# Kernel optimization log

Measured on AMD Instinct MI355X. Metric: run time of the kernel, lower is better.

Reference implementation:

```python
import jax, jax.numpy as jnp
import numpy as np

B, T, D, H = 64, 512, 1024, 1024


def setup_inputs() -> dict:
    key = jax.random.key(0)
    k1, k2, k3, k4, k5, k6 = jax.random.split(key, 6)
    feature = jax.random.normal(k1, (B, T, D), dtype=jnp.float32)
    # lengths sorted descending (pack_padded_sequence enforce_sorted=True); max == T
    lens = jnp.sort(jax.random.randint(k2, (B,), 1, T + 1))[::-1]
    seq_len = lens.at[0].set(T).astype(jnp.int32)
    s = 1.0 / np.sqrt(H)
    W_ih = jax.random.uniform(k3, (4 * H, D), jnp.float32, -s, s)
    W_hh = jax.random.uniform(k4, (4 * H, H), jnp.float32, -s, s)
    b_ih = jax.random.uniform(k5, (4 * H,), jnp.float32, -s, s)
    b_hh = jax.random.uniform(k6, (4 * H,), jnp.float32, -s, s)
    return {"feature": feature, "W_ih": W_ih, "W_hh": W_hh,
            "b_ih": b_ih, "b_hh": b_hh, "seq_len": seq_len}


def _lstm(feature, W_ih, W_hh, b_ih, b_hh, seq_len):
    Bb, Tt, _ = feature.shape
    Hh = W_hh.shape[1]
    # precompute input contributions for all steps: [B,T,4H] -> [T,B,4H]
    x_gates = jnp.einsum('btd,gd->btg', feature, W_ih) + (b_ih + b_hh)
    x_gates = jnp.transpose(x_gates, (1, 0, 2))
    # valid-step mask per timestep: [T,B]
    mask = (jnp.arange(Tt)[:, None] < seq_len[None, :])

    def step(carry, inp):
        h, c = carry
        xg, m = inp  # [B,4H], [B]
        gates = xg + h @ W_hh.T
        i, f, g, o = jnp.split(gates, 4, axis=-1)  # PyTorch gate order i,f,g,o
        i = jax.nn.sigmoid(i)
        f = jax.nn.sigmoid(f)
        g = jnp.tanh(g)
        o = jax.nn.sigmoid(o)
        c_new = f * c + i * g
        h_new = o * jnp.tanh(c_new)
        m = m[:, None]
        h = jnp.where(m, h_new, h)  # packed semantics: state frozen past length
        c = jnp.where(m, c_new, c)
        out = jnp.where(m, h_new, 0.0)  # pad_packed_sequence pads with zeros
        return (h, c), out

    h0 = jnp.zeros((Bb, Hh), feature.dtype)
    c0 = jnp.zeros((Bb, Hh), feature.dtype)
    _, outs = jax.lax.scan(step, (h0, c0), (x_gates, mask))
    return jnp.transpose(outs, (1, 0, 2))  # [B,T,H]


def reference(feature, W_ih, W_hh, b_ih, b_hh, seq_len):
    return _lstm(feature, W_ih, W_hh, b_ih, b_hh, seq_len)
```

## Files before the change

kernel.cpp:

```cpp
#include <hip/hip_runtime.h>
#include <stdint.h>

typedef unsigned short ushort_t;
typedef unsigned long long ull_t;
typedef __attribute__((ext_vector_type(8))) short short8;
typedef __attribute__((ext_vector_type(2))) unsigned long long ull2;
typedef __attribute__((ext_vector_type(4))) float f32x4;
typedef __attribute__((ext_vector_type(4))) float float4v;
typedef __attribute__((ext_vector_type(4))) unsigned short ushort4v;
typedef __attribute__((ext_vector_type(4))) unsigned int uint4v;

#define NB 64
#define NT 512
#define ND 1024
#define NHH 1024
#define NG 4096

__device__ __forceinline__ ushort_t f2bf(float x) {
    uint32_t u = __builtin_bit_cast(uint32_t, x);
    u += 0x7fffu + ((u >> 16) & 1u);
    return (ushort_t)(u >> 16);
}
__device__ __forceinline__ float bf2f(ushort_t b) {
    uint32_t u = ((uint32_t)b) << 16;
    return __builtin_bit_cast(float, u);
}
__device__ __forceinline__ float fsigmoid(float x) { return 1.f / (1.f + __expf(-x)); }
__device__ __forceinline__ float ftanh(float x) {
    float ax = __builtin_fabsf(x);
    float e = __expf(-2.f * ax);
    float r = (1.f - e) / (1.f + e);
    return x < 0.f ? -r : r;
}
__device__ __forceinline__ void xg_store(float* p, float v) { *p = v; }
__device__ __forceinline__ void xg_store(ushort_t* p, float v) { *p = f2bf(v); }
__device__ __forceinline__ float4v xg_load4(const float4v* p) { return *p; }
__device__ __forceinline__ float4v xg_load4(const ushort4v* p) {
    ushort4v u = *p;
    float4v r = { bf2f(u[0]), bf2f(u[1]), bf2f(u[2]), bf2f(u[3]) };
    return r;
}
__device__ __forceinline__ void async_cp16(const ushort_t* g, ushort_t* s) {
    __builtin_amdgcn_global_load_lds(
        (const __attribute__((address_space(1))) uint32_t*)g,
        (__attribute__((address_space(3))) uint32_t*)s, 16, 0, 0);
}

__global__ __launch_bounds__(256) void k_prep(
    const float* __restrict__ feat, const float* __restrict__ wih,
    const float* __restrict__ whh,
    ushort_t* __restrict__ featb, ushort_t* __restrict__ wihb,
    ushort_t* __restrict__ whhb, ushort_t* __restrict__ hbuf,
    int* __restrict__ cnt)
{
    const size_t NF = (size_t)NB * NT * ND / 4;
    const size_t NW = (size_t)NG * ND / 4;
    const size_t NHB = (size_t)2 * 65536 * 2 / 16;
    size_t total = NF + 2 * NW + NHB;
    size_t stride = (size_t)gridDim.x * blockDim.x;
    for (size_t i = (size_t)blockIdx.x * blockDim.x + threadIdx.x; i < total; i += stride) {
        if (i < NF) {
            float4v v = ((const float4v*)feat)[i];
            ushort4v o = { f2bf(v[0]), f2bf(v[1]), f2bf(v[2]), f2bf(v[3]) };
            ((ushort4v*)featb)[i] = o;
        } else if (i < NF + NW) {
            size_t j = i - NF;
            size_t row = j >> 8, kc = j & 255;
            size_t rowp = ((row & 1023) << 2) | (row >> 10);
            float4v v = ((const float4v*)wih)[j];
            ushort4v o = { f2bf(v[0]), f2bf(v[1]), f2bf(v[2]), f2bf(v[3]) };
            ((ushort4v*)wihb)[rowp * 256 + kc] = o;
        } else if (i < NF + 2 * NW) {
            size_t j = i - NF - NW;
            float4v v = ((const float4v*)whh)[j];
            ushort4v o = { f2bf(v[0]), f2bf(v[1]), f2bf(v[2]), f2bf(v[3]) };
            ((ushort4v*)whhb)[j] = o;
        } else {
            size_t j = i - NF - 2 * NW;
            uint4v z = { 0u, 0u, 0u, 0u };
            ((uint4v*)hbuf)[j] = z;
        }
    }
    if (blockIdx.x < 16) cnt[blockIdx.x * 256 + threadIdx.x] = 0;
}

template <typename XGT>
__global__ __launch_bounds__(256) void k_gemm(
    const ushort_t* __restrict__ Ab,
    const ushort_t* __restrict__ Bb,
    const float* __restrict__ bih, const float* __restrict__ bhh,
    const int* __restrict__ slenp, XGT* __restrict__ xg)
{
    int bid = blockIdx.x;
    int panel = bid >> 8;
    int qq = bid & 255;
    int mt = (panel << 3) | (qq & 7);
    int nt = qq >> 3;
    int m0 = mt << 7, n0 = nt << 7;
    int b = m0 >> 9;
    int t0 = m0 & 511;
    int sl = slenp[b];
    if (t0 >= sl) return;

    __shared__ short8 ldsA8[1024];
    __shared__ short8 ldsB8[1024];
    ushort_t* ldsA = (ushort_t*)ldsA8;
    ushort_t* ldsB = (ushort_t*)ldsB8;
    const ushort_t* gA = Ab + (size_t)m0 * 1024;
    const ushort_t* gB = Bb + (size_t)n0 * 1024;

    int tid = threadIdx.x;
    int wave = tid >> 6, lane = tid & 63;
    int wm = (wave >> 1) << 6;
    int wn = (wave & 1) << 6;
    int fl = lane & 15, fq = lane >> 4;

    f32x4 acc[4][4];
#pragma unroll
    for (int i = 0; i < 4; i++)
#pragma unroll
        for (int j = 0; j < 4; j++) { f32x4 z = {0.f, 0.f, 0.f, 0.f}; acc[i][j] = z; }

    int srow_[4], skb_[4];
#pragma unroll
    for (int u = 0; u < 4; u++) {
        int s = u * 256 + tid;
        srow_[u] = s >> 3;
        skb_[u] = (s & 7) ^ (srow_[u] & 7);
    }

    for (int k0 = 0; k0 < 1024; k0 += 64) {
        if (k0) __syncthreads();
#pragma unroll
        for (int u = 0; u < 4; u++) {
            ushort_t* sa = ldsA + (size_t)(u * 256 + wave * 64) * 8;
            ushort_t* sb = ldsB + (size_t)(u * 256 + wave * 64) * 8;
            async_cp16(gA + (size_t)srow_[u] * 1024 + k0 + skb_[u] * 8, sa);
            async_cp16(gB + (size_t)srow_[u] * 1024 + k0 + skb_[u] * 8, sb);
        }
        __syncthreads();
#pragma unroll
        for (int ks = 0; ks < 2; ks++) {
            int kc = ks * 4 + fq;
            short8 af[4], bf[4];
#pragma unroll
            for (int i = 0; i < 4; i++) {
                int ra = wm + i * 16 + fl;
                int rb = wn + i * 16 + fl;
                af[i] = ldsA8[ra * 8 + (kc ^ (ra & 7))];
                bf[i] = ldsB8[rb * 8 + (kc ^ (rb & 7))];
            }
#pragma unroll
            for (int i = 0; i < 4; i++)
#pragma unroll
                for (int j = 0; j < 4; j++)
                    acc[i][j] = __builtin_amdgcn_mfma_f32_16x16x32_bf16(af[i], bf[j], acc[i][j], 0, 0, 0);
        }
    }
#pragma unroll
    for (int j = 0; j < 4; j++) {
        int rp = n0 + wn + j * 16 + fl;
        int bi = ((rp & 3) << 10) | (rp >> 2);
        float bv = bih[bi] + bhh[bi];
#pragma unroll
        for (int i = 0; i < 4; i++) {
#pragma unroll
            for (int r = 0; r < 4; r++) {
                int m = wm + i * 16 + fq * 4 + r;
                int t = t0 + m;
                if (t < sl)
                    xg_store(&xg[((size_t)t * 64 + b) * 4096 + rp], acc[i][j][r] + bv);
            }
        }
    }
}

template <typename XG4>
__global__ __launch_bounds__(256, 1) void k_rec(
    const ushort_t* __restrict__ whhb, const XG4* __restrict__ xg4,
    const int* __restrict__ slenp, ushort_t* __restrict__ hbuf,
    float* __restrict__ out, int* __restrict__ cnt)
{
    const int tid = threadIdx.x;
    const int ks = tid >> 6, lane = tid & 63;
    const int wg = blockIdx.x;
    const int mb = wg >> 6;
    const int mem = wg & 63;
    const int j0 = mem << 4;
    const int nn = lane & 15, q = lane >> 4;

    short8 wfrag[4][8];
    {
        const short8* w8 = (const short8*)whhb;
#pragma unroll
        for (int g = 0; g < 4; g++) {
            const short8* wp = w8 + (size_t)(g * NHH + j0 + nn) * 128 + ks * 32;
#pragma unroll
            for (int u = 0; u < 8; u++) wfrag[g][u] = wp[u * 4 + q];
        }
    }
    const int eb = tid >> 4, ej = tid & 15;
    const int b_g = (mb << 4) + eb;
    const int j_g = j0 + ej;
    const int slen = slenp[b_g];
    const int blk_len = slenp[mb << 4];
    const int ab = (mb << 4) + nn;

    int* base    = cnt + mb * 512;
    int* subcnt  = base + (mem >> 3) * 16;
    int* root    = base + 256;
    int* subflag = base + 272 + (mem >> 3) * 16;
    const bool subleader = ((mem & 7) == 0);

    __shared__ float red[4 * 16 * 84];

    float c_st = 0.f, h_st = 0.f, hv_prev = 0.f;
    float4v xv = { 0.f, 0.f, 0.f, 0.f };
    if (0 < slen) xv = xg_load4(&xg4[(size_t)b_g * 1024 + j_g]);

#pragma unroll 1
    for (int t = 0; t < blk_len; ++t) {
        if (t > 0) out[((size_t)b_g * NT + (t - 1)) * 1024 + j_g] = hv_prev;
        float4v nxv = { 0.f, 0.f, 0.f, 0.f };
        if (t + 1 < slen) nxv = xg_load4(&xg4[((size_t)(t + 1) * 64 + b_g) * 1024 + j_g]);

        const ull_t* hb8 = (const ull_t*)(hbuf + (size_t)(t & 1) * 65536);
        ull_t raw[16];
#pragma unroll
        for (int u = 0; u < 8; u++) {
            size_t ch = ((size_t)((ks * 32 + u * 4 + q) * 64 + ab)) * 2;
            raw[2 * u]     = __hip_atomic_load(&hb8[ch],     __ATOMIC_RELAXED, __HIP_MEMORY_SCOPE_AGENT);
            raw[2 * u + 1] = __hip_atomic_load(&hb8[ch + 1], __ATOMIC_RELAXED, __HIP_MEMORY_SCOPE_AGENT);
        }
        f32x4 acc[4];
#pragma unroll
        for (int g = 0; g < 4; g++) { f32x4 z = {0.f, 0.f, 0.f, 0.f}; acc[g] = z; }
#pragma unroll
        for (int u = 0; u < 8; u++) {
            ull2 p; p[0] = raw[2 * u]; p[1] = raw[2 * u + 1];
            short8 af = __builtin_bit_cast(short8, p);
#pragma unroll
            for (int g = 0; g < 4; g++)
                acc[g] = __builtin_amdgcn_mfma_f32_16x16x32_bf16(af, wfrag[g][u], acc[g], 0, 0, 0);
        }
        __syncthreads();
#pragma unroll
        for (int g = 0; g < 4; g++)
            *(f32x4*)&red[g * 1344 + nn * 84 + ks * 20 + q * 4] = acc[g];
        __syncthreads();

        float hv = 0.f;
        if (t < slen) {
            float s[4];
#pragma unroll
            for (int g = 0; g < 4; g++) {
                const float* rp = &red[g * 1344 + ej * 84 + eb];
                s[g] = (rp[0] + rp[20]) + (rp[40] + rp[60]);
            }
            float ip = s[0] + xv[0];
            float fp = s[1] + xv[1];
            float gp = s[2] + xv[2];
            float op = s[3] + xv[3];
            float i_s = fsigmoid(ip), f_s = fsigmoid(fp);
            float g_t = ftanh(gp), o_s = fsigmoid(op);
            float cn = __builtin_fmaf(f_s, c_st, i_s * g_t);
            c_st = cn;
            h_st = o_s * ftanh(cn);
            hv = h_st;
        }
        hv_prev = hv;
        __hip_atomic_store(&hbuf[(size_t)((t + 1) & 1) * 65536 +
                                 (size_t)((j_g >> 3) * 64 + b_g) * 8 + (j_g & 7)],
                           f2bf(h_st), __ATOMIC_RELAXED, __HIP_MEMORY_SCOPE_AGENT);
        xv = nxv;
        if (t + 1 < blk_len) {
            asm volatile("s_waitcnt vmcnt(0)" ::: "memory");
            __syncthreads();
            if (tid == 0) {
                int old = __hip_atomic_fetch_add(subcnt, 1, __ATOMIC_RELAXED, __HIP_MEMORY_SCOPE_AGENT);
                if ((old & 7) == 7)
                    __hip_atomic_fetch_add(root, 1, __ATOMIC_RELAXED, __HIP_MEMORY_SCOPE_AGENT);
                const int target = (t + 1) << 3;
                if (subleader) {
                    while (__hip_atomic_load(root, __ATOMIC_RELAXED, __HIP_MEMORY_SCOPE_AGENT) < target)
                        __builtin_amdgcn_s_sleep(2);
                    __hip_atomic_store(subflag, t + 1, __ATOMIC_RELAXED, __HIP_MEMORY_SCOPE_AGENT);
                } else {
                    while (__hip_atomic_load(subflag, __ATOMIC_RELAXED, __HIP_MEMORY_SCOPE_AGENT) < t + 1)
                        __builtin_amdgcn_s_sleep(2);
                }
            }
            __syncthreads();
        }
    }
    out[((size_t)b_g * NT + (blk_len - 1)) * 1024 + j_g] = hv_prev;
    for (int t = blk_len; t < NT; ++t)
        out[((size_t)b_g * NT + t) * 1024 + j_g] = 0.f;
}

extern "C" void kernel_launch(void* const* d_in, const int* in_sizes, int n_in,
                              void* d_out, int out_size, void* d_ws, size_t ws_size,
                              hipStream_t stream)
{
    const float* feat = (const float*)d_in[0];
    const float* wih  = (const float*)d_in[1];
    const float* whh  = (const float*)d_in[2];
    const float* bih  = (const float*)d_in[3];
    const float* bhh  = (const float*)d_in[4];
    const int*   sl   = (const int*)d_in[5];
    float* out = (float*)d_out;
    char* ws = (char*)d_ws;

    size_t off = 0;
    auto take = [&](size_t bytes) -> size_t {
        size_t o = off; off += (bytes + 255) & ~(size_t)255; return o;
    };
    size_t o_featb = take((size_t)NB * NT * ND * 2);
    size_t o_wihb  = take((size_t)NG * ND * 2);
    size_t o_whhb  = take((size_t)NG * ND * 2);
    size_t o_hbuf  = take((size_t)2 * 65536 * 2);
    size_t o_cnt   = take(16384);
    size_t o_xg    = off;

    ushort_t* featb = (ushort_t*)(ws + o_featb);
    ushort_t* wihb  = (ushort_t*)(ws + o_wihb);
    ushort_t* whhb  = (ushort_t*)(ws + o_whhb);
    ushort_t* hbuf  = (ushort_t*)(ws + o_hbuf);
    int* cnt        = (int*)(ws + o_cnt);

    k_prep<<<2048, 256, 0, stream>>>(feat, wih, whh, featb, wihb, whhb, hbuf, cnt);

    size_t xg_elems = (size_t)NT * NB * NG;
    bool f32xg = (o_xg + xg_elems * 4) <= ws_size;
    if (f32xg) {
        float* xg = (float*)(ws + o_xg);
        k_gemm<float><<<8192, 256, 0, stream>>>(featb, wihb, bih, bhh, sl, xg);
        k_rec<float4v><<<256, 256, 0, stream>>>(whhb, (const float4v*)xg, sl, hbuf, out, cnt);
    } else {
        ushort_t* xg = (ushort_t*)(ws + o_xg);
        k_gemm<ushort_t><<<8192, 256, 0, stream>>>(featb, wihb, bih, bhh, sl, xg);
        k_rec<ushort4v><<<256, 256, 0, stream>>>(whhb, (const ushort4v*)xg, sl, hbuf, out, cnt);
    }
}
```

Baseline: 2.608 ms.

## Widen recurrence blocks to 32 hidden units and flatten grid barrier

Each recurrent workgroup now covers 32 hidden columns with 8 waves (512 threads), which halves the grid to 128 blocks and the number of participants per batch group to 32. The per-step h exchange is staged through shared memory, and one wave writes it out as packed 16-byte stores in a new per-batch-group-contiguous layout, replacing scattered 2-byte atomic stores. The two-level subcounter/root/subflag barrier is replaced by a single flat counter per batch group. The intent is to cut per-step global sync latency and store traffic. The cost is more contention on one counter and an extra block-wide sync per step.

```diff
diff --git a/kernel.cpp b/kernel.cpp
--- a/kernel.cpp
+++ b/kernel.cpp
@@ -176,43 +176,40 @@
 }
 
 template <typename XG4>
-__global__ __launch_bounds__(256, 1) void k_rec(
+__global__ __launch_bounds__(512, 2) void k_rec(
     const ushort_t* __restrict__ whhb, const XG4* __restrict__ xg4,
     const int* __restrict__ slenp, ushort_t* __restrict__ hbuf,
     float* __restrict__ out, int* __restrict__ cnt)
 {
     const int tid = threadIdx.x;
-    const int ks = tid >> 6, lane = tid & 63;
+    const int wave = tid >> 6, lane = tid & 63;
+    const int ks = wave >> 1, jb = wave & 1;
     const int wg = blockIdx.x;
-    const int mb = wg >> 6;
-    const int mem = wg & 63;
-    const int j0 = mem << 4;
+    const int mb = wg >> 5;
+    const int jw = wg & 31;
     const int nn = lane & 15, q = lane >> 4;
 
     short8 wfrag[4][8];
     {
         const short8* w8 = (const short8*)whhb;
+        const int jr = jw * 32 + jb * 16 + nn;
 #pragma unroll
         for (int g = 0; g < 4; g++) {
-            const short8* wp = w8 + (size_t)(g * NHH + j0 + nn) * 128 + ks * 32;
+            const short8* wp = w8 + (size_t)(g * NHH + jr) * 128 + ks * 32;
 #pragma unroll
             for (int u = 0; u < 8; u++) wfrag[g][u] = wp[u * 4 + q];
         }
     }
-    const int eb = tid >> 4, ej = tid & 15;
+    const int eb = tid >> 5, ej = tid & 31;
     const int b_g = (mb << 4) + eb;
-    const int j_g = j0 + ej;
+    const int j_g = jw * 32 + ej;
     const int slen = slenp[b_g];
     const int blk_len = slenp[mb << 4];
-    const int ab = (mb << 4) + nn;
-
-    int* base    = cnt + mb * 512;
-    int* subcnt  = base + (mem >> 3) * 16;
-    int* root    = base + 256;
-    int* subflag = base + 272 + (mem >> 3) * 16;
-    const bool subleader = ((mem & 7) == 0);
-
-    __shared__ float red[4 * 16 * 84];
+
+    int* cnt_mb = cnt + mb * 64;
+
+    __shared__ float red[4 * 32 * 84];
+    __shared__ ushort_t htile[16 * 40];
 
     float c_st = 0.f, h_st = 0.f, hv_prev = 0.f;
     float4v xv = { 0.f, 0.f, 0.f, 0.f };
@@ -224,11 +221,11 @@
         float4v nxv = { 0.f, 0.f, 0.f, 0.f };
         if (t + 1 < slen) nxv = xg_load4(&xg4[((size_t)(t + 1) * 64 + b_g) * 1024 + j_g]);
 
-        const ull_t* hb8 = (const ull_t*)(hbuf + (size_t)(t & 1) * 65536);
+        const ull_t* hb8 = (const ull_t*)hbuf + (size_t)(t & 1) * 16384;
         ull_t raw[16];
 #pragma unroll
         for (int u = 0; u < 8; u++) {
-            size_t ch = ((size_t)((ks * 32 + u * 4 + q) * 64 + ab)) * 2;
+            size_t ch = (size_t)(mb * 2048 + (ks * 32 + u * 4 + q) * 16 + nn) * 2;
             raw[2 * u]     = __hip_atomic_load(&hb8[ch],     __ATOMIC_RELAXED, __HIP_MEMORY_SCOPE_AGENT);
             raw[2 * u + 1] = __hip_atomic_load(&hb8[ch + 1], __ATOMIC_RELAXED, __HIP_MEMORY_SCOPE_AGENT);
         }
@@ -246,7 +243,7 @@
         __syncthreads();
 #pragma unroll
         for (int g = 0; g < 4; g++)
-            *(f32x4*)&red[g * 1344 + nn * 84 + ks * 20 + q * 4] = acc[g];
+            *(f32x4*)&red[g * 2688 + (jb * 16 + nn) * 84 + ks * 20 + q * 4] = acc[g];
         __syncthreads();
 
         float hv = 0.f;
@@ -254,7 +251,7 @@
             float s[4];
 #pragma unroll
             for (int g = 0; g < 4; g++) {
-                const float* rp = &red[g * 1344 + ej * 84 + eb];
+                const float* rp = &red[g * 2688 + ej * 84 + eb];
                 s[g] = (rp[0] + rp[20]) + (rp[40] + rp[60]);
             }
             float ip = s[0] + xv[0];
@@ -269,25 +266,24 @@
             hv = h_st;
         }
         hv_prev = hv;
-        __hip_atomic_store(&hbuf[(size_t)((t + 1) & 1) * 65536 +
-                                 (size_t)((j_g >> 3) * 64 + b_g) * 8 + (j_g & 7)],
-                           f2bf(h_st), __ATOMIC_RELAXED, __HIP_MEMORY_SCOPE_AGENT);
         xv = nxv;
+        htile[eb * 40 + ej] = f2bf(h_st);
+        __syncthreads();
+
         if (t + 1 < blk_len) {
-            asm volatile("s_waitcnt vmcnt(0)" ::: "memory");
-            __syncthreads();
-            if (tid == 0) {
-                int old = __hip_atomic_fetch_add(subcnt, 1, __ATOMIC_RELAXED, __HIP_MEMORY_SCOPE_AGENT);
-                if ((old & 7) == 7)
-                    __hip_atomic_fetch_add(root, 1, __ATOMIC_RELAXED, __HIP_MEMORY_SCOPE_AGENT);
-                const int target = (t + 1) << 3;
-                if (subleader) {
-                    while (__hip_atomic_load(root, __ATOMIC_RELAXED, __HIP_MEMORY_SCOPE_AGENT) < target)
-                        __builtin_amdgcn_s_sleep(2);
-                    __hip_atomic_store(subflag, t + 1, __ATOMIC_RELAXED, __HIP_MEMORY_SCOPE_AGENT);
-                } else {
-                    while (__hip_atomic_load(subflag, __ATOMIC_RELAXED, __HIP_MEMORY_SCOPE_AGENT) < t + 1)
-                        __builtin_amdgcn_s_sleep(2);
+            if (wave == 0) {
+                short8 hv8 = *(const short8*)&htile[(lane & 15) * 40 + (lane >> 4) * 8];
+                ull2 pk = __builtin_bit_cast(ull2, hv8);
+                ull_t* dst = (ull_t*)hbuf + (size_t)((t + 1) & 1) * 16384 +
+                             (size_t)(mb * 2048 + jw * 64 + lane) * 2;
+                __hip_atomic_store(&dst[0], pk[0], __ATOMIC_RELAXED, __HIP_MEMORY_SCOPE_AGENT);
+                __hip_atomic_store(&dst[1], pk[1], __ATOMIC_RELAXED, __HIP_MEMORY_SCOPE_AGENT);
+                asm volatile("s_waitcnt vmcnt(0)" ::: "memory");
+                if (lane == 0) {
+                    __hip_atomic_fetch_add(cnt_mb, 1, __ATOMIC_RELAXED, __HIP_MEMORY_SCOPE_AGENT);
+                    const int target = (t + 1) << 5;
+                    while (__hip_atomic_load(cnt_mb, __ATOMIC_RELAXED, __HIP_MEMORY_SCOPE_AGENT) < target)
+                        __builtin_amdgcn_s_sleep(1);
                 }
             }
             __syncthreads();
@@ -335,10 +331,10 @@
     if (f32xg) {
         float* xg = (float*)(ws + o_xg);
         k_gemm<float><<<8192, 256, 0, stream>>>(featb, wihb, bih, bhh, sl, xg);
-        k_rec<float4v><<<256, 256, 0, stream>>>(whhb, (const float4v*)xg, sl, hbuf, out, cnt);
+        k_rec<float4v><<<128, 512, 0, stream>>>(whhb, (const float4v*)xg, sl, hbuf, out, cnt);
     } else {
         ushort_t* xg = (ushort_t*)(ws + o_xg);
         k_gemm<ushort_t><<<8192, 256, 0, stream>>>(featb, wihb, bih, bhh, sl, xg);
-        k_rec<ushort4v><<<256, 256, 0, stream>>>(whhb, (const ushort4v*)xg, sl, hbuf, out, cnt);
-    }
-}
+        k_rec<ushort4v><<<128, 512, 0, stream>>>(whhb, (const ushort4v*)xg, sl, hbuf, out, cnt);
+    }
+}
```

New measurement: 2.870 ms. +10.0%, slower.
